# Performance work log

Hardware: AMD Instinct MI355X
Metric: run time of the kernel (lower is better)

Reference implementation:

```python
import jax, jax.numpy as jnp
import numpy as np

S = 30.0
M = 0.4
B, D, C = 1024, 512, 100000


def setup_inputs() -> dict:
    key = jax.random.key(0)
    kx, kw, kl = jax.random.split(key, 3)
    x = jax.random.normal(kx, (B, D), dtype=jnp.float32)
    # nn.Parameter init: uniform(-1,1); the renorm-to-unit-columns happens in forward
    W = jax.random.uniform(kw, (D, C), dtype=jnp.float32, minval=-1.0, maxval=1.0)
    label = jax.random.randint(kl, (B,), 0, C).astype(jnp.int64)
    return {"x": x, "W": W, "label": label}


def reference(x, W, label):
    # F.normalize(x, dim=1): L2-normalize rows (eps=1e-12 clamp on the norm)
    X = x / jnp.clip(jnp.linalg.norm(x, axis=1, keepdims=True), 1e-12)
    # W.renorm(2,1,1e-5).mul_(1e5): columns renormed to norm 1e-5 then scaled by 1e5
    # -> effectively unit-norm columns (all random columns have norm >> 1e-5)
    Wn = W / jnp.clip(jnp.linalg.norm(W, axis=0, keepdims=True), 1e-12)
    cossim = jnp.clip(X @ Wn, -1.0, 1.0)                      # [B, C]
    tgt = jnp.take_along_axis(cossim, label[:, None], axis=1)[:, 0]  # [B]
    numerator = S * (tgt - M)                                  # [B]
    # sum over all non-label classes of exp(s*cos) == full sum minus label term
    excl_sum = jnp.sum(jnp.exp(S * cossim), axis=1) - jnp.exp(S * tgt)
    L = numerator - jnp.log(jnp.exp(numerator) + excl_sum)
    return cossim, -jnp.mean(L)
```

## Files before the change

### kernel.cpp

```cpp
#include <hip/hip_runtime.h>
#include <hip/hip_bf16.h>
#include <cstdint>
#include <cstddef>

constexpr int   Bm = 1024;
constexpr int   Dk = 512;
constexpr int   Cn = 100000;
constexpr float S_SCALE = 30.0f;
constexpr float MARGIN  = 0.4f;

static_assert(Cn % 4 == 0, "N must be multiple of 4 for float4 loads");

typedef __bf16 bf16_t;
typedef __bf16 bf16x4 __attribute__((ext_vector_type(4)));
typedef __bf16 bf16x8 __attribute__((ext_vector_type(8)));
typedef float  f32x4  __attribute__((ext_vector_type(4)));

constexpr int BN    = 128;
constexpr int BK    = 32;
constexpr int NSTEP = Dk / BK;
constexpr int NT    = (Cn + BN - 1) / BN;
constexpr int NTP   = 784;
constexpr int LDB   = 40;

__global__ __launch_bounds__(64) void k_prep_x(const float* __restrict__ x,
                                               bf16_t* __restrict__ Xbf) {
    const int row  = blockIdx.x;
    const int lane = threadIdx.x;
    const float* xp = x + (size_t)row * Dk + lane * 8;
    float4 a = *(const float4*)xp;
    float4 b = *(const float4*)(xp + 4);
    float s = a.x*a.x + a.y*a.y + a.z*a.z + a.w*a.w
            + b.x*b.x + b.y*b.y + b.z*b.z + b.w*b.w;
    #pragma unroll
    for (int off = 1; off < 64; off <<= 1) s += __shfl_xor(s, off);
    const float inv = rsqrtf(fmaxf(s, 1e-24f));
    bf16x8 v;
    v[0] = (bf16_t)(a.x * inv); v[1] = (bf16_t)(a.y * inv);
    v[2] = (bf16_t)(a.z * inv); v[3] = (bf16_t)(a.w * inv);
    v[4] = (bf16_t)(b.x * inv); v[5] = (bf16_t)(b.y * inv);
    v[6] = (bf16_t)(b.z * inv); v[7] = (bf16_t)(b.w * inv);
    *(bf16x8*)(Xbf + (size_t)row * Dk + lane * 8) = v;
}

__global__ __launch_bounds__(256) void k_gemm(const float* __restrict__ W,
                                              const bf16_t* __restrict__ Xbf,
                                              float* __restrict__ out,
                                              float* __restrict__ part) {
    __shared__ bf16_t Blds[BN * LDB];
    __shared__ float  nsqbuf[BN * 8];
    __shared__ float  wninv[BN];
    __shared__ float  rsbuf[128 * 2];

    const int id    = blockIdx.x;
    const int nt    = (id >> 6) * 8 + (id & 7);
    const int mt8   = (id >> 3) & 7;
    if (nt >= NT) return;
    const int n0 = nt * BN;
    const int m0 = mt8 * 128;

    const int tid  = threadIdx.x;
    const int wave = tid >> 6, lane = tid & 63;
    const int wm   = wave >> 1, wn = wave & 1;
    const int quad = lane >> 4, l16 = lane & 15;

    const int ng = tid >> 3, kg = tid & 7;
    const int n_loc = ng * 4, k_loc = kg * 4;
    const bool svalid = (n0 + n_loc) < Cn;
    const float* wrow = W + (size_t)k_loc * Cn + (n0 + n_loc);

    f32x4 acc[4][4];
    #pragma unroll
    for (int i = 0; i < 4; ++i)
        #pragma unroll
        for (int j = 0; j < 4; ++j) acc[i][j] = (f32x4){0.f, 0.f, 0.f, 0.f};

    float nsq0 = 0.f, nsq1 = 0.f, nsq2 = 0.f, nsq3 = 0.f;

    const float4 fz = make_float4(0.f, 0.f, 0.f, 0.f);
    float4 r0 = fz, r1 = fz, r2 = fz, r3 = fz;
    if (svalid) {
        r0 = *(const float4*)(wrow);
        r1 = *(const float4*)(wrow + (size_t)Cn);
        r2 = *(const float4*)(wrow + (size_t)2 * Cn);
        r3 = *(const float4*)(wrow + (size_t)3 * Cn);
    }

    const bf16_t* abase = Xbf + (size_t)(m0 + wm * 64 + l16) * Dk + quad * 8;

    #pragma unroll 2
    for (int step = 0; step < NSTEP; ++step) {
        __syncthreads();
        nsq0 += r0.x*r0.x + r1.x*r1.x + r2.x*r2.x + r3.x*r3.x;
        nsq1 += r0.y*r0.y + r1.y*r1.y + r2.y*r2.y + r3.y*r3.y;
        nsq2 += r0.z*r0.z + r1.z*r1.z + r2.z*r2.z + r3.z*r3.z;
        nsq3 += r0.w*r0.w + r1.w*r1.w + r2.w*r2.w + r3.w*r3.w;
        {
            bf16x4 p;
            p[0]=(bf16_t)r0.x; p[1]=(bf16_t)r1.x; p[2]=(bf16_t)r2.x; p[3]=(bf16_t)r3.x;
            *(bf16x4*)&Blds[(n_loc + 0) * LDB + k_loc] = p;
            p[0]=(bf16_t)r0.y; p[1]=(bf16_t)r1.y; p[2]=(bf16_t)r2.y; p[3]=(bf16_t)r3.y;
            *(bf16x4*)&Blds[(n_loc + 1) * LDB + k_loc] = p;
            p[0]=(bf16_t)r0.z; p[1]=(bf16_t)r1.z; p[2]=(bf16_t)r2.z; p[3]=(bf16_t)r3.z;
            *(bf16x4*)&Blds[(n_loc + 2) * LDB + k_loc] = p;
            p[0]=(bf16_t)r0.w; p[1]=(bf16_t)r1.w; p[2]=(bf16_t)r2.w; p[3]=(bf16_t)r3.w;
            *(bf16x4*)&Blds[(n_loc + 3) * LDB + k_loc] = p;
        }
        __syncthreads();

        float4 q0 = fz, q1 = fz, q2 = fz, q3 = fz;
        if ((step + 1 < NSTEP) && svalid) {
            const float* pp = wrow + (size_t)((step + 1) * BK) * Cn;
            q0 = *(const float4*)(pp);
            q1 = *(const float4*)(pp + (size_t)Cn);
            q2 = *(const float4*)(pp + (size_t)2 * Cn);
            q3 = *(const float4*)(pp + (size_t)3 * Cn);
        }

        const bf16_t* ab = abase + step * BK;
        bf16x8 af[4];
        #pragma unroll
        for (int mt = 0; mt < 4; ++mt)
            af[mt] = *(const bf16x8*)(ab + (size_t)mt * 16 * Dk);
        bf16x8 bfr[4];
        #pragma unroll
        for (int nl = 0; nl < 4; ++nl)
            bfr[nl] = *(const bf16x8*)&Blds[(wn * 64 + nl * 16 + l16) * LDB + quad * 8];

        #pragma unroll
        for (int mt = 0; mt < 4; ++mt)
            #pragma unroll
            for (int nl = 0; nl < 4; ++nl)
                acc[mt][nl] = __builtin_amdgcn_mfma_f32_16x16x32_bf16(
                    af[mt], bfr[nl], acc[mt][nl], 0, 0, 0);

        r0 = q0; r1 = q1; r2 = q2; r3 = q3;
    }

    __syncthreads();
    nsqbuf[(n_loc + 0) * 8 + kg] = nsq0;
    nsqbuf[(n_loc + 1) * 8 + kg] = nsq1;
    nsqbuf[(n_loc + 2) * 8 + kg] = nsq2;
    nsqbuf[(n_loc + 3) * 8 + kg] = nsq3;
    __syncthreads();
    if (tid < BN) {
        float s = 0.f;
        #pragma unroll
        for (int i = 0; i < 8; ++i) s += nsqbuf[tid * 8 + i];
        wninv[tid] = rsqrtf(fmaxf(s, 1e-24f));
    }
    __syncthreads();

    float eacc[4][4];
    #pragma unroll
    for (int i = 0; i < 4; ++i)
        #pragma unroll
        for (int j = 0; j < 4; ++j) eacc[i][j] = 0.f;

    #pragma unroll
    for (int mt = 0; mt < 4; ++mt) {
        const int mrow = m0 + wm * 64 + mt * 16 + quad * 4;
        #pragma unroll
        for (int nl = 0; nl < 4; ++nl) {
            const int ncol = wn * 64 + nl * 16 + l16;
            const int n = n0 + ncol;
            if (n < Cn) {
                const float inv = wninv[ncol];
                #pragma unroll
                for (int reg = 0; reg < 4; ++reg) {
                    float v = acc[mt][nl][reg] * inv;
                    v = fminf(fmaxf(v, -1.f), 1.f);
                    out[(size_t)(mrow + reg) * Cn + n] = v;
                    eacc[mt][reg] += __expf(S_SCALE * v);
                }
            }
        }
    }
    #pragma unroll
    for (int mt = 0; mt < 4; ++mt)
        #pragma unroll
        for (int reg = 0; reg < 4; ++reg) {
            float e = eacc[mt][reg];
            #pragma unroll
            for (int off = 1; off < 16; off <<= 1) e += __shfl_xor(e, off);
            if (l16 == 0)
                rsbuf[(wm * 64 + mt * 16 + quad * 4 + reg) * 2 + wn] = e;
        }
    __syncthreads();
    if (tid < 128)
        part[(size_t)(m0 + tid) * NTP + nt] = rsbuf[tid * 2] + rsbuf[tid * 2 + 1];
}

__global__ __launch_bounds__(256) void k_row(const float* __restrict__ part,
                                             const float* __restrict__ out,
                                             const int* __restrict__ label,
                                             float* __restrict__ Lbuf) {
    const int b = blockIdx.x, tid = threadIdx.x;
    float s = 0.f;
    const float* p = part + (size_t)b * NTP;
    for (int i = tid; i < NT; i += 256) s += p[i];
    #pragma unroll
    for (int off = 1; off < 64; off <<= 1) s += __shfl_xor(s, off);
    __shared__ float wsum[4];
    if ((tid & 63) == 0) wsum[tid >> 6] = s;
    __syncthreads();
    if (tid == 0) {
        const float rowsum = wsum[0] + wsum[1] + wsum[2] + wsum[3];
        const int c = label[b];
        const float tgt = out[(size_t)b * Cn + c];
        const float num = S_SCALE * (tgt - MARGIN);
        const float excl = rowsum - __expf(S_SCALE * tgt);
        Lbuf[b] = num - __logf(__expf(num) + excl);
    }
}

__global__ __launch_bounds__(256) void k_loss(const float* __restrict__ Lbuf,
                                              float* __restrict__ out) {
    const int tid = threadIdx.x;
    float s = 0.f;
    for (int i = tid; i < Bm; i += 256) s += Lbuf[i];
    #pragma unroll
    for (int off = 1; off < 64; off <<= 1) s += __shfl_xor(s, off);
    __shared__ float wsum[4];
    if ((tid & 63) == 0) wsum[tid >> 6] = s;
    __syncthreads();
    if (tid == 0)
        out[(size_t)Bm * Cn] = -(wsum[0] + wsum[1] + wsum[2] + wsum[3]) / (float)Bm;
}

extern "C" void kernel_launch(void* const* d_in, const int* in_sizes, int n_in,
                              void* d_out, int out_size, void* d_ws, size_t ws_size,
                              hipStream_t stream) {
    const float* x     = (const float*)d_in[0];
    const float* W     = (const float*)d_in[1];
    const int*   label = (const int*)d_in[2];
    float* out = (float*)d_out;

    bf16_t* Xbf = (bf16_t*)d_ws;
    float*  part = (float*)((char*)d_ws + (1 << 20));
    float*  Lbuf = (float*)((char*)d_ws + (1 << 20) + (size_t)Bm * NTP * 4);

    k_prep_x<<<Bm, 64, 0, stream>>>(x, Xbf);
    k_gemm<<<98 * 64, 256, 0, stream>>>(W, Xbf, out, part);
    k_row<<<Bm, 256, 0, stream>>>(part, out, label, Lbuf);
    k_loss<<<1, 256, 0, stream>>>(Lbuf, out);
}
```

Measured before the change: 929.2 us.

## Pre-normalize W to transposed bf16 and stage GEMM tiles via global_load_lds

Adds a prep kernel that computes column norms of W once, normalizes and converts it to a transposed bf16 buffer in workspace, using a swizzled LDS transpose. The GEMM then streams the bf16 tiles directly into LDS with global_load_lds in 64-wide K steps, using an XOR swizzle instead of padding. This removes the redundant fp32 W reads and in-kernel conversion that each of the 8 M-tiles previously repeated. The cost is an extra pass over W, about 100 MB of workspace, and a fallback path if the workspace is too small.

```diff
diff --git a/kernel.cpp b/kernel.cpp
--- a/kernel.cpp
+++ b/kernel.cpp
@@ -17,11 +17,17 @@
 typedef float  f32x4  __attribute__((ext_vector_type(4)));
 
 constexpr int BN    = 128;
-constexpr int BK    = 32;
-constexpr int NSTEP = Dk / BK;
 constexpr int NT    = (Cn + BN - 1) / BN;
 constexpr int NTP   = 784;
-constexpr int LDB   = 40;
+
+constexpr size_t WBFT_B    = (size_t)Cn * Dk * 2;
+constexpr size_t XBF_B     = (size_t)Bm * Dk * 2;
+constexpr size_t PART_B    = (size_t)Bm * NTP * 4;
+constexpr size_t NEED_FAST = WBFT_B + XBF_B + PART_B + 4096;
+
+constexpr int BK_L    = 32;
+constexpr int NSTEP_L = Dk / BK_L;
+constexpr int LDB_L   = 40;
 
 __global__ __launch_bounds__(64) void k_prep_x(const float* __restrict__ x,
                                                bf16_t* __restrict__ Xbf) {
@@ -43,11 +49,187 @@
     *(bf16x8*)(Xbf + (size_t)row * Dk + lane * 8) = v;
 }
 
-__global__ __launch_bounds__(256) void k_gemm(const float* __restrict__ W,
+constexpr int PC = 64;
+__global__ __launch_bounds__(256) void k_prep_w(const float* __restrict__ W,
+                                                bf16_t* __restrict__ WbfT) {
+    __shared__ alignas(16) bf16_t T[PC * Dk];
+    __shared__ float nsqb[PC][4];
+    __shared__ float invn[PC];
+
+    const int c0  = blockIdx.x * PC;
+    const int t   = threadIdx.x;
+    const int col = t & 63, kg = t >> 6;
+    const int c   = c0 + col;
+    const bool cv = c < Cn;
+    const float* p = W + (size_t)(kg * 128) * Cn + c;
+
+    float nsq = 0.f;
+    if (cv) {
+        #pragma unroll 8
+        for (int i = 0; i < 128; ++i) {
+            const float v = p[(size_t)i * Cn];
+            nsq += v * v;
+        }
+    }
+    nsqb[col][kg] = nsq;
+    __syncthreads();
+    if (t < PC)
+        invn[t] = rsqrtf(fmaxf(nsqb[t][0] + nsqb[t][1] + nsqb[t][2] + nsqb[t][3], 1e-24f));
+    __syncthreads();
+
+    const float inv = invn[col];
+    if (cv) {
+        #pragma unroll 2
+        for (int s = 0; s < 16; ++s) {
+            bf16x8 v;
+            #pragma unroll
+            for (int j = 0; j < 8; ++j)
+                v[j] = (bf16_t)(p[(size_t)(s * 8 + j) * Cn] * inv);
+            const int slot = (kg * 16 + s) ^ (col & 7);
+            *(bf16x8*)&T[col * Dk + slot * 8] = v;
+        }
+    }
+    __syncthreads();
+
+    const int wv = t >> 6, l = t & 63;
+    #pragma unroll 4
+    for (int rr = 0; rr < 16; ++rr) {
+        const int r  = wv * 16 + rr;
+        const int cc = c0 + r;
+        if (cc < Cn) {
+            bf16x8 v = *(const bf16x8*)&T[r * Dk + ((l ^ (r & 7)) * 8)];
+            *(bf16x8*)(WbfT + (size_t)cc * Dk + l * 8) = v;
+        }
+    }
+}
+
+__global__ __launch_bounds__(256) void k_gemm(const bf16_t* __restrict__ WbfT,
                                               const bf16_t* __restrict__ Xbf,
                                               float* __restrict__ out,
                                               float* __restrict__ part) {
-    __shared__ bf16_t Blds[BN * LDB];
+    __shared__ alignas(16) bf16_t Blds[BN * 64];
+    __shared__ float rsbuf[128 * 2];
+
+    const int id  = blockIdx.x;
+    const int nt  = (id >> 6) * 8 + (id & 7);
+    const int mt8 = (id >> 3) & 7;
+    if (nt >= NT) return;
+    const int n0 = nt * BN;
+    const int m0 = mt8 * 128;
+
+    const int tid  = threadIdx.x;
+    const int wave = tid >> 6, lane = tid & 63;
+    const int wm   = wave >> 1, wn = wave & 1;
+    const int quad = lane >> 4, l16 = lane & 15;
+
+    const int sh = lane >> 3, sl = lane & 7;
+    const int srcslot = sl ^ sh;
+    const bf16_t* ssrc[4];
+    #pragma unroll
+    for (int it = 0; it < 4; ++it) {
+        int r = n0 + it * 32 + wave * 8 + sh;
+        r = (r < Cn) ? r : (Cn - 1);
+        ssrc[it] = WbfT + (size_t)r * Dk + srcslot * 8;
+    }
+    bf16_t* sdst = &Blds[wave * 512];
+
+    #define STAGE(koff) do {                                                        \
+        _Pragma("unroll")                                                           \
+        for (int it_ = 0; it_ < 4; ++it_)                                           \
+            __builtin_amdgcn_global_load_lds(                                       \
+                (const __attribute__((address_space(1))) void*)(ssrc[it_] + (koff)),\
+                (__attribute__((address_space(3))) void*)(sdst + it_ * 2048),       \
+                16, 0, 0);                                                          \
+    } while (0)
+
+    f32x4 acc[4][4];
+    #pragma unroll
+    for (int i = 0; i < 4; ++i)
+        #pragma unroll
+        for (int j = 0; j < 4; ++j) acc[i][j] = (f32x4){0.f, 0.f, 0.f, 0.f};
+
+    const bf16_t* abase = Xbf + (size_t)(m0 + wm * 64 + l16) * Dk + quad * 8;
+
+    STAGE(0);
+    for (int step = 0; step < 8; ++step) {
+        __syncthreads();
+
+        bf16x8 bfr[4][2];
+        #pragma unroll
+        for (int nl = 0; nl < 4; ++nl) {
+            const int rn = wn * 64 + nl * 16 + l16;
+            #pragma unroll
+            for (int kk = 0; kk < 2; ++kk) {
+                const int slot = (kk * 4 + quad) ^ (rn & 7);
+                bfr[nl][kk] = *(const bf16x8*)&Blds[rn * 64 + slot * 8];
+            }
+        }
+        bf16x8 af[4][2];
+        #pragma unroll
+        for (int mt = 0; mt < 4; ++mt)
+            #pragma unroll
+            for (int kk = 0; kk < 2; ++kk)
+                af[mt][kk] = *(const bf16x8*)(abase + step * 64 + kk * 32
+                                              + (size_t)mt * 16 * Dk);
+
+        __syncthreads();
+        if (step < 7) STAGE((step + 1) * 64);
+
+        #pragma unroll
+        for (int kk = 0; kk < 2; ++kk)
+            #pragma unroll
+            for (int mt = 0; mt < 4; ++mt)
+                #pragma unroll
+                for (int nl = 0; nl < 4; ++nl)
+                    acc[mt][nl] = __builtin_amdgcn_mfma_f32_16x16x32_bf16(
+                        af[mt][kk], bfr[nl][kk], acc[mt][nl], 0, 0, 0);
+    }
+    #undef STAGE
+
+    float eacc[4][4];
+    #pragma unroll
+    for (int i = 0; i < 4; ++i)
+        #pragma unroll
+        for (int j = 0; j < 4; ++j) eacc[i][j] = 0.f;
+
+    #pragma unroll
+    for (int mt = 0; mt < 4; ++mt) {
+        const int mrow = m0 + wm * 64 + mt * 16 + quad * 4;
+        #pragma unroll
+        for (int nl = 0; nl < 4; ++nl) {
+            const int ncol = wn * 64 + nl * 16 + l16;
+            const int n = n0 + ncol;
+            if (n < Cn) {
+                #pragma unroll
+                for (int reg = 0; reg < 4; ++reg) {
+                    float v = acc[mt][nl][reg];
+                    v = fminf(fmaxf(v, -1.f), 1.f);
+                    out[(size_t)(mrow + reg) * Cn + n] = v;
+                    eacc[mt][reg] += __expf(S_SCALE * v);
+                }
+            }
+        }
+    }
+    #pragma unroll
+    for (int mt = 0; mt < 4; ++mt)
+        #pragma unroll
+        for (int reg = 0; reg < 4; ++reg) {
+            float e = eacc[mt][reg];
+            #pragma unroll
+            for (int off = 1; off < 16; off <<= 1) e += __shfl_xor(e, off);
+            if (l16 == 0)
+                rsbuf[(wm * 64 + mt * 16 + quad * 4 + reg) * 2 + wn] = e;
+        }
+    __syncthreads();
+    if (tid < 128)
+        part[(size_t)(m0 + tid) * NTP + nt] = rsbuf[tid * 2] + rsbuf[tid * 2 + 1];
+}
+
+__global__ __launch_bounds__(256) void k_gemm_legacy(const float* __restrict__ W,
+                                                     const bf16_t* __restrict__ Xbf,
+                                                     float* __restrict__ out,
+                                                     float* __restrict__ part) {
+    __shared__ bf16_t Blds[BN * LDB_L];
     __shared__ float  nsqbuf[BN * 8];
     __shared__ float  wninv[BN];
     __shared__ float  rsbuf[128 * 2];
@@ -89,7 +271,7 @@
     const bf16_t* abase = Xbf + (size_t)(m0 + wm * 64 + l16) * Dk + quad * 8;
 
     #pragma unroll 2
-    for (int step = 0; step < NSTEP; ++step) {
+    for (int step = 0; step < NSTEP_L; ++step) {
         __syncthreads();
         nsq0 += r0.x*r0.x + r1.x*r1.x + r2.x*r2.x + r3.x*r3.x;
         nsq1 += r0.y*r0.y + r1.y*r1.y + r2.y*r2.y + r3.y*r3.y;
@@ -98,26 +280,26 @@
         {
             bf16x4 p;
             p[0]=(bf16_t)r0.x; p[1]=(bf16_t)r1.x; p[2]=(bf16_t)r2.x; p[3]=(bf16_t)r3.x;
-            *(bf16x4*)&Blds[(n_loc + 0) * LDB + k_loc] = p;
+            *(bf16x4*)&Blds[(n_loc + 0) * LDB_L + k_loc] = p;
             p[0]=(bf16_t)r0.y; p[1]=(bf16_t)r1.y; p[2]=(bf16_t)r2.y; p[3]=(bf16_t)r3.y;
-            *(bf16x4*)&Blds[(n_loc + 1) * LDB + k_loc] = p;
+            *(bf16x4*)&Blds[(n_loc + 1) * LDB_L + k_loc] = p;
             p[0]=(bf16_t)r0.z; p[1]=(bf16_t)r1.z; p[2]=(bf16_t)r2.z; p[3]=(bf16_t)r3.z;
-            *(bf16x4*)&Blds[(n_loc + 2) * LDB + k_loc] = p;
+            *(bf16x4*)&Blds[(n_loc + 2) * LDB_L + k_loc] = p;
             p[0]=(bf16_t)r0.w; p[1]=(bf16_t)r1.w; p[2]=(bf16_t)r2.w; p[3]=(bf16_t)r3.w;
-            *(bf16x4*)&Blds[(n_loc + 3) * LDB + k_loc] = p;
+            *(bf16x4*)&Blds[(n_loc + 3) * LDB_L + k_loc] = p;
         }
         __syncthreads();
 
         float4 q0 = fz, q1 = fz, q2 = fz, q3 = fz;
-        if ((step + 1 < NSTEP) && svalid) {
-            const float* pp = wrow + (size_t)((step + 1) * BK) * Cn;
+        if ((step + 1 < NSTEP_L) && svalid) {
+            const float* pp = wrow + (size_t)((step + 1) * BK_L) * Cn;
             q0 = *(const float4*)(pp);
             q1 = *(const float4*)(pp + (size_t)Cn);
             q2 = *(const float4*)(pp + (size_t)2 * Cn);
             q3 = *(const float4*)(pp + (size_t)3 * Cn);
         }
 
-        const bf16_t* ab = abase + step * BK;
+        const bf16_t* ab = abase + step * BK_L;
         bf16x8 af[4];
         #pragma unroll
         for (int mt = 0; mt < 4; ++mt)
@@ -125,7 +307,7 @@
         bf16x8 bfr[4];
         #pragma unroll
         for (int nl = 0; nl < 4; ++nl)
-            bfr[nl] = *(const bf16x8*)&Blds[(wn * 64 + nl * 16 + l16) * LDB + quad * 8];
+            bfr[nl] = *(const bf16x8*)&Blds[(wn * 64 + nl * 16 + l16) * LDB_L + quad * 8];
 
         #pragma unroll
         for (int mt = 0; mt < 4; ++mt)
@@ -236,12 +418,25 @@
     const int*   label = (const int*)d_in[2];
     float* out = (float*)d_out;
 
-    bf16_t* Xbf = (bf16_t*)d_ws;
-    float*  part = (float*)((char*)d_ws + (1 << 20));
-    float*  Lbuf = (float*)((char*)d_ws + (1 << 20) + (size_t)Bm * NTP * 4);
-
-    k_prep_x<<<Bm, 64, 0, stream>>>(x, Xbf);
-    k_gemm<<<98 * 64, 256, 0, stream>>>(W, Xbf, out, part);
-    k_row<<<Bm, 256, 0, stream>>>(part, out, label, Lbuf);
-    k_loss<<<1, 256, 0, stream>>>(Lbuf, out);
-}
+    if (ws_size >= NEED_FAST) {
+        bf16_t* WbfT = (bf16_t*)d_ws;
+        bf16_t* Xbf  = (bf16_t*)((char*)d_ws + WBFT_B);
+        float*  part = (float*)((char*)d_ws + WBFT_B + XBF_B);
+        float*  Lbuf = (float*)((char*)d_ws + WBFT_B + XBF_B + PART_B);
+
+        k_prep_x<<<Bm, 64, 0, stream>>>(x, Xbf);
+        k_prep_w<<<(Cn + PC - 1) / PC, 256, 0, stream>>>(W, WbfT);
+        k_gemm<<<98 * 64, 256, 0, stream>>>(WbfT, Xbf, out, part);
+        k_row<<<Bm, 256, 0, stream>>>(part, out, label, Lbuf);
+        k_loss<<<1, 256, 0, stream>>>(Lbuf, out);
+    } else {
+        bf16_t* Xbf  = (bf16_t*)d_ws;
+        float*  part = (float*)((char*)d_ws + (1 << 20));
+        float*  Lbuf = (float*)((char*)d_ws + (1 << 20) + (size_t)Bm * NTP * 4);
+
+        k_prep_x<<<Bm, 64, 0, stream>>>(x, Xbf);
+        k_gemm_legacy<<<98 * 64, 256, 0, stream>>>(W, Xbf, out, part);
+        k_row<<<Bm, 256, 0, stream>>>(part, out, label, Lbuf);
+        k_loss<<<1, 256, 0, stream>>>(Lbuf, out);
+    }
+}
```

Result: faster. 880.1 us (-5.3%).
